# Performance work log

Measured on AMD Instinct MI355X. Metric: run time of the kernel, lower is better.

Reference implementation:

```python
import jax, jax.numpy as jnp
import numpy as np

HIDDEN = 1024
HEADS = 16
DEPTH = HIDDEN // HEADS  # 64
B, S = 1, 2048  # batch must be 1: E is built with shape (heads, B*S, depth) and the skew reshape assumes B*S == S


def setup_inputs() -> dict:
    key = jax.random.key(0)
    ks = jax.random.split(key, 6)
    std = 0.02
    x = jax.random.normal(ks[0], (B, S, HIDDEN), dtype=jnp.float32)
    c_attn_w = jax.random.normal(ks[1], (HIDDEN, 3 * HIDDEN), dtype=jnp.float32) * std
    c_attn_b = jnp.zeros((1, 3 * HIDDEN), dtype=jnp.float32)
    c_proj_w = jax.random.normal(ks[2], (HIDDEN, HIDDEN), dtype=jnp.float32) * std
    c_proj_b = jnp.zeros((1, HIDDEN), dtype=jnp.float32)
    # GlorotUniform for E of shape (heads, B*S, depth)
    limit = float(np.sqrt(6.0 / (B * S + DEPTH)))
    E = jax.random.uniform(ks[3], (HEADS, B * S, DEPTH), dtype=jnp.float32,
                           minval=-limit, maxval=limit)
    return {"x": x, "c_attn_w": c_attn_w, "c_attn_b": c_attn_b,
            "c_proj_w": c_proj_w, "c_proj_b": c_proj_b, "E": E}


def _split_heads(t):
    # [B,S,H] -> [B,heads,S,depth]
    b, s, h = t.shape
    return t.reshape(b, s, HEADS, h // HEADS).transpose(0, 2, 1, 3)


def _relative_attention(q, E):
    # Transformer-XL style skewing. q: [B,heads,S,depth], E: [heads,B*S,depth]
    b, h, s, d = q.shape
    q_ = q.transpose(1, 0, 2, 3).reshape(h, b * s, d)
    rel = jnp.einsum('hnd,hmd->hnm', q_, E)            # [h, B*S, B*S]
    rel = rel.reshape(h, b, s, s)
    rel = jnp.pad(rel, ((0, 0), (0, 0), (0, 0), (1, 0)))  # pad left on last dim
    rel = rel.reshape(h, b, s + 1, s)[:, :, 1:]            # skew
    return rel.transpose(1, 0, 2, 3)                       # [B,heads,S,S]


def reference(x, c_attn_w, c_attn_b, c_proj_w, c_proj_b, E):
    b, s, hidden = x.shape
    qkv = x @ c_attn_w + c_attn_b                      # [B,S,3H]
    q, k, v = jnp.split(qkv, 3, axis=2)
    q, k, v = _split_heads(q), _split_heads(k), _split_heads(v)  # [B,h,S,d]

    w = jnp.einsum('bhqd,bhkd->bhqk', q, k)            # raw scores
    w = w + _relative_attention(q, E)
    w = w * jax.lax.rsqrt(jnp.asarray(DEPTH, w.dtype))  # scale applied after rel bias

    # causal mask: 1 in lower triangle (i >= j - ns + nd, nd == ns == S)
    i = jnp.arange(s)[:, None]
    j = jnp.arange(s)[None, :]
    bmask = (i >= j).astype(w.dtype)[None, None]        # [1,1,S,S]
    w = w * bmask - 10000.0 * (1.0 - bmask)

    a = jax.nn.softmax(w, axis=-1)                      # dropout is identity at inference
    ctx = jnp.einsum('bhqk,bhkd->bhqd', a, v)
    ctx = ctx.transpose(0, 2, 1, 3).reshape(b, s, hidden)  # merge heads
    out = ctx @ c_proj_w + c_proj_b
    return out
```

## Files before the change

kernel.cpp:

```cpp
#include <hip/hip_runtime.h>
#include <math.h>

#define SEQ  2048
#define NH   16
#define DEP  64
#define HID  1024

typedef __attribute__((ext_vector_type(8))) short s16x8;
typedef __attribute__((ext_vector_type(4))) float f32x4;

#define MFMA16(a, b, c) __builtin_amdgcn_mfma_f32_16x16x32_bf16(a, b, c, 0, 0, 0)
#define GLDS16(g, l)                                                           \
  __builtin_amdgcn_global_load_lds(                                            \
      (const __attribute__((address_space(1))) void*)(g),                      \
      (__attribute__((address_space(3))) void*)(l), 16, 0, 0)

__device__ __forceinline__ ushort f2b(float f) {
  union { float f; unsigned u; } x; x.f = f;
  unsigned r = (x.u + 0x7fff + ((x.u >> 16) & 1)) >> 16;
  return (ushort)r;
}
__device__ __forceinline__ float b2f(ushort u) {
  union { unsigned u; float f; } x; x.u = ((unsigned)u) << 16;
  return x.f;
}

__global__ __launch_bounds__(256) void prep(
    const float* __restrict__ x, ushort* __restrict__ xb,
    const float* __restrict__ E, ushort* __restrict__ Eb,
    const float* __restrict__ Wa, ushort* __restrict__ Wat,
    const float* __restrict__ Wp, ushort* __restrict__ Wpt) {
  const int bid = blockIdx.x, t = threadIdx.x;
  if (bid < 1024) {
    __shared__ float Ls[64 * 68];
    const float* in; ushort* out; int C, tile;
    if (bid < 768) { in = Wa; out = Wat; C = 3072; tile = bid; }
    else           { in = Wp; out = Wpt; C = 1024; tile = bid - 768; }
    const int ntx = C / 64;
    const int n0 = (tile % ntx) * 64, k0 = (tile / ntx) * 64;
    const int r = t >> 4, c4 = t & 15;
    #pragma unroll
    for (int p = 0; p < 4; p++) {
      float4 v = *(const float4*)&in[(size_t)(k0 + r + 16 * p) * C + n0 + c4 * 4];
      *(float4*)&Ls[(r + 16 * p) * 68 + c4 * 4] = v;
    }
    __syncthreads();
    #pragma unroll
    for (int p = 0; p < 4; p++) {
      int rw = r + 16 * p;
      ushort4 o;
      o.x = f2b(Ls[(c4 * 4 + 0) * 68 + rw]);
      o.y = f2b(Ls[(c4 * 4 + 1) * 68 + rw]);
      o.z = f2b(Ls[(c4 * 4 + 2) * 68 + rw]);
      o.w = f2b(Ls[(c4 * 4 + 3) * 68 + rw]);
      *(ushort4*)&out[(size_t)(n0 + rw) * 1024 + k0 + c4 * 4] = o;
    }
  } else {
    const int id = bid - 1024;
    #pragma unroll
    for (int rep = 0; rep < 4; rep++) {
      int i = id * 256 + t + rep * 262144;
      const float* src; ushort* dst; int k;
      if (i < 524288) { src = x; dst = xb; k = i; }
      else            { src = E; dst = Eb; k = i - 524288; }
      float4 v = *(const float4*)&src[(size_t)k * 4];
      ushort4 o = {f2b(v.x), f2b(v.y), f2b(v.z), f2b(v.w)};
      *(ushort4*)&dst[(size_t)k * 4] = o;
    }
  }
}

template <int MODE>
__global__ __launch_bounds__(256, 3) void gemm_mfma(
    const ushort* __restrict__ A, const ushort* __restrict__ Bt,
    const float* __restrict__ bias, int N, int K,
    ushort* __restrict__ qd, ushort* __restrict__ kd, ushort* __restrict__ vt,
    float* __restrict__ Cout) {
  __shared__ ushort As[2][64 * 64];
  __shared__ ushort Bs[2][128 * 64];
  const int t = threadIdx.x, l = t & 63, w = t >> 6;
  const int lr = l & 15, quad = l >> 4;
  const int row8 = l >> 3;
  const int chunk = (l & 7) ^ ((l >> 3) & 7);
  const int m0 = blockIdx.y * 64, n0 = blockIdx.x * 128;
  const int wr = (w >> 1) * 32, wc = (w & 1) * 64;
  f32x4 acc[2][4] = {};
  const ushort* gA = A + (size_t)m0 * K + chunk * 8;
  const ushort* gB = Bt + (size_t)n0 * K + chunk * 8;

  auto issue = [&](int buf, int k0) {
    #pragma unroll
    for (int g = 0; g < 2; g++) {
      int r = 16 * w + 8 * g + row8;
      GLDS16(gA + (size_t)r * K + k0, &As[buf][(16 * w + 8 * g) * 64]);
    }
    #pragma unroll
    for (int g = 0; g < 4; g++) {
      int r = 32 * w + 8 * g + row8;
      GLDS16(gB + (size_t)r * K + k0, &Bs[buf][(32 * w + 8 * g) * 64]);
    }
  };

  issue(0, 0);
  const int nsteps = K / 64;
  for (int s = 0; s < nsteps; s++) {
    __syncthreads();
    if (s + 1 < nsteps) issue((s + 1) & 1, (s + 1) * 64);
    const char* as_ = (const char*)As[s & 1];
    const char* bs_ = (const char*)Bs[s & 1];
    s16x8 af[2][2], bf[4][2];
    #pragma unroll
    for (int i = 0; i < 2; i++)
      #pragma unroll
      for (int hh = 0; hh < 2; hh++)
        af[i][hh] = *(const s16x8*)(as_ + (wr + 16 * i + lr) * 128 +
                                    (((4 * hh + quad) ^ (lr & 7)) * 16));
    #pragma unroll
    for (int j = 0; j < 4; j++)
      #pragma unroll
      for (int hh = 0; hh < 2; hh++)
        bf[j][hh] = *(const s16x8*)(bs_ + (wc + 16 * j + lr) * 128 +
                                    (((4 * hh + quad) ^ (lr & 7)) * 16));
    #pragma unroll
    for (int i = 0; i < 2; i++)
      #pragma unroll
      for (int j = 0; j < 4; j++) {
        acc[i][j] = MFMA16(af[i][0], bf[j][0], acc[i][j]);
        acc[i][j] = MFMA16(af[i][1], bf[j][1], acc[i][j]);
      }
  }

  #pragma unroll
  for (int i = 0; i < 2; i++) {
    #pragma unroll
    for (int j = 0; j < 4; j++) {
      const int colg = n0 + wc + 16 * j + lr;
      const float bb = bias[colg];
      const int rowg0 = m0 + wr + 16 * i + 4 * quad;
      if (MODE == 0) {
        const int part = colg >> 10, hh = (colg >> 6) & 15, d = colg & 63;
        if (part == 2) {
          ushort4 ov;
          ov.x = f2b(acc[i][j][0] + bb);
          ov.y = f2b(acc[i][j][1] + bb);
          ov.z = f2b(acc[i][j][2] + bb);
          ov.w = f2b(acc[i][j][3] + bb);
          *(ushort4*)&vt[((size_t)hh * 64 + d) * SEQ + rowg0] = ov;
        } else {
          ushort* dst = part == 0 ? qd : kd;
          const float sc = part == 0 ? 0.125f : 1.0f;
          #pragma unroll
          for (int r = 0; r < 4; r++)
            dst[((size_t)hh * SEQ + rowg0 + r) * 64 + d] = f2b((acc[i][j][r] + bb) * sc);
        }
      } else {
        #pragma unroll
        for (int r = 0; r < 4; r++)
          Cout[(size_t)(rowg0 + r) * N + colg] = acc[i][j][r] + bb;
      }
    }
  }
}

__global__ __launch_bounds__(256, 2) void attn_mfma(
    const ushort* __restrict__ qw, const ushort* __restrict__ kw,
    const ushort* __restrict__ vT, const ushort* __restrict__ Ebf,
    ushort* __restrict__ ctx, ushort* __restrict__ pa_o,
    float* __restrict__ pa_l) {
  __shared__ ushort KT[2][64 * 64];
  __shared__ ushort VS[2][64 * 64];
  __shared__ ushort EB[2][128 * 64];
  __shared__ ushort PB[4][16 * 72];
  const int t = threadIdx.x, l = t & 63, w = t >> 6;
  const int lr = l & 15, quad = l >> 4;
  const int row8 = l >> 3;
  const int chunk = (l & 7) ^ ((l >> 3) & 7);
  const int h = blockIdx.y;
  const int p = blockIdx.x >> 1, half = blockIdx.x & 1;
  const int i0A = 64 * p, i0B = 64 * (31 - p);

  int ph_i0[2], ph_k0[2], ph_k1[2], nph, tot;
  bool ph_diag[2], ph_dir[2];
  if (half == 0) {
    ph_i0[0] = i0A; ph_k0[0] = 0; ph_k1[0] = p + 1;  ph_diag[0] = true;  ph_dir[0] = true;
    ph_i0[1] = i0B; ph_k0[1] = 0; ph_k1[1] = 16 - p; ph_diag[1] = false; ph_dir[1] = false;
    nph = 2; tot = 17;
  } else {
    ph_i0[0] = i0B; ph_k0[0] = 16 - p; ph_k1[0] = 32 - p; ph_diag[0] = true; ph_dir[0] = false;
    ph_i0[1] = 0; ph_k0[1] = 0; ph_k1[1] = 0; ph_diag[1] = false; ph_dir[1] = false;
    nph = 1; tot = 16;
  }

  const ushort* kwh = kw + (size_t)h * SEQ * 64;
  const ushort* vgh = vT + (size_t)h * 64 * SEQ;
  const ushort* egh = Ebf + (size_t)h * SEQ * 64;

  auto issue = [&](int buf, int i0_, int j0) {
    const int m0 = 1984 - i0_ + j0;
    const ushort* kb = kwh + (size_t)j0 * 64 + chunk * 8;
    const ushort* vb = vgh + j0 + chunk * 8;
    #pragma unroll
    for (int g = 0; g < 2; g++) {
      int r = 16 * w + 8 * g + row8;
      GLDS16(kb + (size_t)r * 64, &KT[buf][(16 * w + 8 * g) * 64]);
      GLDS16(vb + (size_t)r * SEQ, &VS[buf][(16 * w + 8 * g) * 64]);
    }
    #pragma unroll
    for (int g = 0; g < 4; g++) {
      int r = m0 + 32 * w + 8 * g + row8;
      if (r > SEQ - 1) r = SEQ - 1;
      GLDS16(egh + (size_t)r * 64 + chunk * 8, &EB[buf][(32 * w + 8 * g) * 64]);
    }
  };

  int pi = 0, kt = ph_k0[0];
  issue(0, ph_i0[0], kt * 64);

  s16x8 aq0, aq1;
  {
    const ushort* qg = qw + ((size_t)h * SEQ + ph_i0[0] + 16 * w) * 64;
    aq0 = *(const s16x8*)(qg + lr * 64 + quad * 8);
    aq1 = *(const s16x8*)(qg + lr * 64 + 32 + quad * 8);
  }

  f32x4 o[4] = {};
  float li[4] = {0.f, 0.f, 0.f, 0.f};
  f32x4 rtc = {};

  for (int s = 0; s < tot; s++) {
    __syncthreads();

    const int i0 = ph_i0[pi];
    const bool first = (kt == ph_k0[pi]);
    const bool last = (kt == ph_k1[pi] - 1);
    const bool diag = ph_diag[pi] && last;

    {
      int npi = pi, nkt = kt + 1;
      bool have = true;
      if (nkt == ph_k1[pi]) {
        if (pi + 1 < nph) { npi = pi + 1; nkt = ph_k0[npi]; } else have = false;
      }
      if (have) issue((s + 1) & 1, ph_i0[npi], nkt * 64);
    }

    const char* KTc = (const char*)KT[s & 1];
    const char* VSc = (const char*)VS[s & 1];
    const char* EBc = (const char*)EB[s & 1];

    f32x4 s4[4];
    #pragma unroll
    for (int b = 0; b < 4; b++) {
      const int row = 16 * b + lr;
      s16x8 bk0 = *(const s16x8*)(KTc + row * 128 + ((quad ^ (lr & 7)) * 16));
      s16x8 bk1 = *(const s16x8*)(KTc + row * 128 + (((4 + quad) ^ (lr & 7)) * 16));
      f32x4 z = {};
      z = MFMA16(aq0, bk0, z);
      z = MFMA16(aq1, bk1, z);
      s4[b] = z;
    }

    {
      const int ebase = 48 - 16 * w;
      f32x4 rt[5];
      if (first) {
        const int row = ebase + lr;
        s16x8 e0 = *(const s16x8*)(EBc + row * 128 + ((quad ^ (lr & 7)) * 16));
        s16x8 e1 = *(const s16x8*)(EBc + row * 128 + (((4 + quad) ^ (lr & 7)) * 16));
        f32x4 z = {};
        z = MFMA16(aq0, e0, z);
        z = MFMA16(aq1, e1, z);
        rt[0] = z;
      } else {
        rt[0] = rtc;
      }
      #pragma unroll
      for (int b = 1; b < 5; b++) {
        const int row = ebase + 16 * b + lr;
        s16x8 e0 = *(const s16x8*)(EBc + row * 128 + ((quad ^ (lr & 7)) * 16));
        s16x8 e1 = *(const s16x8*)(EBc + row * 128 + (((4 + quad) ^ (lr & 7)) * 16));
        f32x4 z = {};
        z = MFMA16(aq0, e0, z);
        z = MFMA16(aq1, e1, z);
        rt[b] = z;
      }
      rtc = rt[4];
      #pragma unroll
      for (int b = 0; b < 4; b++)
        #pragma unroll
        for (int r = 0; r < 4; r++) {
          int ti = 4 * quad + r;
          int u = lr - ti + 15;
          int src = (u & 15) | (l & 48);
          float v0 = __shfl(rt[b][r], src);
          float v1 = __shfl(rt[b + 1][r], src);
          s4[b][r] += (u < 16) ? v0 : v1;
        }
    }

    if (diag) {
      #pragma unroll
      for (int b = 0; b < 4; b++)
        #pragma unroll
        for (int r = 0; r < 4; r++) {
          int ii = 16 * w + 4 * quad + r;
          if (16 * b + lr > ii) s4[b][r] = -10000.0f;
        }
    }

    #pragma unroll
    for (int b = 0; b < 4; b++)
      #pragma unroll
      for (int r = 0; r < 4; r++) {
        float pp = __expf(s4[b][r]);
        s4[b][r] = pp;
        li[r] += pp;
      }

    {
      char* Pw = (char*)PB[w];
      #pragma unroll
      for (int b = 0; b < 4; b++)
        #pragma unroll
        for (int r = 0; r < 4; r++)
          *(ushort*)(Pw + (4 * quad + r) * 144 + (16 * b + lr) * 2) = f2b(s4[b][r]);
      s16x8 pa0 = *(const s16x8*)(Pw + lr * 144 + quad * 16);
      s16x8 pa1 = *(const s16x8*)(Pw + lr * 144 + 64 + quad * 16);
      #pragma unroll
      for (int dc = 0; dc < 4; dc++) {
        const int row = 16 * dc + lr;
        s16x8 bv0 = *(const s16x8*)(VSc + row * 128 + ((quad ^ (lr & 7)) * 16));
        s16x8 bv1 = *(const s16x8*)(VSc + row * 128 + (((4 + quad) ^ (lr & 7)) * 16));
        o[dc] = MFMA16(pa0, bv0, o[dc]);
        o[dc] = MFMA16(pa1, bv1, o[dc]);
      }
    }

    if (last) {
      float lsum[4];
      #pragma unroll
      for (int r = 0; r < 4; r++) {
        float v = li[r];
        v += __shfl_xor(v, 1);
        v += __shfl_xor(v, 2);
        v += __shfl_xor(v, 4);
        v += __shfl_xor(v, 8);
        lsum[r] = v;
      }
      if (ph_dir[pi]) {
        #pragma unroll
        for (int r = 0; r < 4; r++) {
          float inv = 1.0f / lsum[r];
          #pragma unroll
          for (int dc = 0; dc < 4; dc++) {
            int row = i0 + 16 * w + 4 * quad + r;
            int col = h * 64 + 16 * dc + lr;
            ctx[(size_t)row * HID + col] = f2b(o[dc][r] * inv);
          }
        }
      } else {
        ushort* po = pa_o + (((size_t)(h * 16 + p) * 2 + half) * 4096);
        float* pl = pa_l + (((size_t)(h * 16 + p) * 2 + half) * 64);
        #pragma unroll
        for (int r = 0; r < 4; r++) {
          int row = 16 * w + 4 * quad + r;
          #pragma unroll
          for (int dc = 0; dc < 4; dc++)
            po[row * 64 + 16 * dc + lr] = f2b(o[dc][r]);
          if (lr == 0) pl[row] = lsum[r];
        }
      }
      #pragma unroll
      for (int dc = 0; dc < 4; dc++) o[dc] = (f32x4){0.f, 0.f, 0.f, 0.f};
      #pragma unroll
      for (int r = 0; r < 4; r++) li[r] = 0.f;
      if (pi + 1 < nph) {
        const ushort* qg = qw + ((size_t)h * SEQ + ph_i0[pi + 1] + 16 * w) * 64;
        aq0 = *(const s16x8*)(qg + lr * 64 + quad * 8);
        aq1 = *(const s16x8*)(qg + lr * 64 + 32 + quad * 8);
      }
    }

    if (kt + 1 == ph_k1[pi]) { pi++; kt = (pi < nph) ? ph_k0[pi] : 0; }
    else kt++;
  }
}

__global__ __launch_bounds__(256) void merge_p(const ushort* __restrict__ pa_o,
                                               const float* __restrict__ pa_l,
                                               ushort* __restrict__ ctx) {
  const int p = blockIdx.x, h = blockIdx.y, t = threadIdx.x;
  const int row = t >> 2, seg = t & 3;
  const ushort* o0 = pa_o + ((size_t)(h * 16 + p) * 2 + 0) * 4096;
  const ushort* o1 = pa_o + ((size_t)(h * 16 + p) * 2 + 1) * 4096;
  const float* l0 = pa_l + ((size_t)(h * 16 + p) * 2 + 0) * 64;
  const float* l1 = pa_l + ((size_t)(h * 16 + p) * 2 + 1) * 64;
  const float inv = 1.0f / (l0[row] + l1[row]);
  const int i0b = 64 * (31 - p);
  #pragma unroll
  for (int g = 0; g < 2; g++) {
    ushort a[8], b[8], r[8];
    *(int4*)a = *(const int4*)&o0[row * 64 + seg * 16 + g * 8];
    *(int4*)b = *(const int4*)&o1[row * 64 + seg * 16 + g * 8];
    #pragma unroll
    for (int j = 0; j < 8; j++) r[j] = f2b((b2f(a[j]) + b2f(b[j])) * inv);
    *(int4*)&ctx[(size_t)(i0b + row) * HID + h * 64 + seg * 16 + g * 8] = *(int4*)r;
  }
}

extern "C" void kernel_launch(void* const* d_in, const int* in_sizes, int n_in,
                              void* d_out, int out_size, void* d_ws, size_t ws_size,
                              hipStream_t stream) {
  (void)in_sizes; (void)n_in; (void)out_size; (void)ws_size;
  const float* x  = (const float*)d_in[0];
  const float* Wa = (const float*)d_in[1];
  const float* ba = (const float*)d_in[2];
  const float* Wp = (const float*)d_in[3];
  const float* bp = (const float*)d_in[4];
  const float* E  = (const float*)d_in[5];
  float* out = (float*)d_out;

  ushort* xb  = (ushort*)d_ws;
  ushort* ctx = xb;
  ushort* Wat = xb + (size_t)2 * 1024 * 1024;
  ushort* Wpt = Wat + (size_t)3 * 1024 * 1024;
  ushort* Ebf = Wpt + (size_t)1024 * 1024;
  ushort* qwp = Ebf + (size_t)2 * 1024 * 1024;
  ushort* kwp = qwp + (size_t)2 * 1024 * 1024;
  ushort* vTp = kwp + (size_t)2 * 1024 * 1024;
  ushort* pa_o = Wat;
  float*  pa_l = (float*)(Wat + (size_t)2 * 1024 * 1024);

  prep<<<2048, 256, 0, stream>>>(x, xb, E, Ebf, Wa, Wat, Wp, Wpt);
  gemm_mfma<0><<<dim3(24, 32), 256, 0, stream>>>(xb, Wat, ba, 3 * HID, HID,
                                                 qwp, kwp, vTp, nullptr);
  attn_mfma<<<dim3(32, NH), 256, 0, stream>>>(qwp, kwp, vTp, Ebf, ctx,
                                              pa_o, pa_l);
  merge_p<<<dim3(16, NH), 256, 0, stream>>>(pa_o, pa_l, ctx);
  gemm_mfma<1><<<dim3(8, 32), 256, 0, stream>>>(ctx, Wpt, bp, HID, HID,
                                                nullptr, nullptr, nullptr, out);
}
```

Before: 160.1 us.

## Reuse overlapping E rows via ring buffer and narrow output-projection GEMM tiles

The attention kernel now keeps E tiles in a 4-slot ring of 64-row slots. Consecutive key tiles share 64 of their 128 skewed E rows, so each step loads only one new 64-row slot instead of the full 128 rows, with two slots loaded when a new phase starts. Separately, the GEMM is templated on tile width, and the output projection uses 64-wide tiles to launch twice as many blocks and fill more CUs. The slot indexing and phase-change logic add complexity, and it could break if the row overlap assumption fails.

```diff
diff --git a/kernel.cpp b/kernel.cpp
--- a/kernel.cpp
+++ b/kernel.cpp
@@ -70,21 +70,22 @@
   }
 }
 
-template <int MODE>
+template <int MODE, int BN>
 __global__ __launch_bounds__(256, 3) void gemm_mfma(
     const ushort* __restrict__ A, const ushort* __restrict__ Bt,
     const float* __restrict__ bias, int N, int K,
     ushort* __restrict__ qd, ushort* __restrict__ kd, ushort* __restrict__ vt,
     float* __restrict__ Cout) {
+  constexpr int NJ = BN / 32;
   __shared__ ushort As[2][64 * 64];
-  __shared__ ushort Bs[2][128 * 64];
+  __shared__ ushort Bs[2][BN * 64];
   const int t = threadIdx.x, l = t & 63, w = t >> 6;
   const int lr = l & 15, quad = l >> 4;
   const int row8 = l >> 3;
   const int chunk = (l & 7) ^ ((l >> 3) & 7);
-  const int m0 = blockIdx.y * 64, n0 = blockIdx.x * 128;
-  const int wr = (w >> 1) * 32, wc = (w & 1) * 64;
-  f32x4 acc[2][4] = {};
+  const int m0 = blockIdx.y * 64, n0 = blockIdx.x * BN;
+  const int wr = (w >> 1) * 32, wc = (w & 1) * (BN / 2);
+  f32x4 acc[2][NJ] = {};
   const ushort* gA = A + (size_t)m0 * K + chunk * 8;
   const ushort* gB = Bt + (size_t)n0 * K + chunk * 8;
 
@@ -95,9 +96,9 @@
       GLDS16(gA + (size_t)r * K + k0, &As[buf][(16 * w + 8 * g) * 64]);
     }
     #pragma unroll
-    for (int g = 0; g < 4; g++) {
-      int r = 32 * w + 8 * g + row8;
-      GLDS16(gB + (size_t)r * K + k0, &Bs[buf][(32 * w + 8 * g) * 64]);
+    for (int g = 0; g < BN / 32; g++) {
+      int r = (BN / 4) * w + 8 * g + row8;
+      GLDS16(gB + (size_t)r * K + k0, &Bs[buf][((BN / 4) * w + 8 * g) * 64]);
     }
   };
 
@@ -108,7 +109,7 @@
     if (s + 1 < nsteps) issue((s + 1) & 1, (s + 1) * 64);
     const char* as_ = (const char*)As[s & 1];
     const char* bs_ = (const char*)Bs[s & 1];
-    s16x8 af[2][2], bf[4][2];
+    s16x8 af[2][2], bf[NJ][2];
     #pragma unroll
     for (int i = 0; i < 2; i++)
       #pragma unroll
@@ -116,7 +117,7 @@
         af[i][hh] = *(const s16x8*)(as_ + (wr + 16 * i + lr) * 128 +
                                     (((4 * hh + quad) ^ (lr & 7)) * 16));
     #pragma unroll
-    for (int j = 0; j < 4; j++)
+    for (int j = 0; j < NJ; j++)
       #pragma unroll
       for (int hh = 0; hh < 2; hh++)
         bf[j][hh] = *(const s16x8*)(bs_ + (wc + 16 * j + lr) * 128 +
@@ -124,7 +125,7 @@
     #pragma unroll
     for (int i = 0; i < 2; i++)
       #pragma unroll
-      for (int j = 0; j < 4; j++) {
+      for (int j = 0; j < NJ; j++) {
         acc[i][j] = MFMA16(af[i][0], bf[j][0], acc[i][j]);
         acc[i][j] = MFMA16(af[i][1], bf[j][1], acc[i][j]);
       }
@@ -133,7 +134,7 @@
   #pragma unroll
   for (int i = 0; i < 2; i++) {
     #pragma unroll
-    for (int j = 0; j < 4; j++) {
+    for (int j = 0; j < NJ; j++) {
       const int colg = n0 + wc + 16 * j + lr;
       const float bb = bias[colg];
       const int rowg0 = m0 + wr + 16 * i + 4 * quad;
@@ -169,7 +170,7 @@
     float* __restrict__ pa_l) {
   __shared__ ushort KT[2][64 * 64];
   __shared__ ushort VS[2][64 * 64];
-  __shared__ ushort EB[2][128 * 64];
+  __shared__ ushort EB[4][64 * 64];
   __shared__ ushort PB[4][16 * 72];
   const int t = threadIdx.x, l = t & 63, w = t >> 6;
   const int lr = l & 15, quad = l >> 4;
@@ -195,8 +196,7 @@
   const ushort* vgh = vT + (size_t)h * 64 * SEQ;
   const ushort* egh = Ebf + (size_t)h * SEQ * 64;
 
-  auto issue = [&](int buf, int i0_, int j0) {
-    const int m0 = 1984 - i0_ + j0;
+  auto issue_kv = [&](int buf, int j0) {
     const ushort* kb = kwh + (size_t)j0 * 64 + chunk * 8;
     const ushort* vb = vgh + j0 + chunk * 8;
     #pragma unroll
@@ -205,16 +205,23 @@
       GLDS16(kb + (size_t)r * 64, &KT[buf][(16 * w + 8 * g) * 64]);
       GLDS16(vb + (size_t)r * SEQ, &VS[buf][(16 * w + 8 * g) * 64]);
     }
-    #pragma unroll
-    for (int g = 0; g < 4; g++) {
-      int r = m0 + 32 * w + 8 * g + row8;
+  };
+  auto issue_e = [&](int slot, int r0) {
+    #pragma unroll
+    for (int g = 0; g < 2; g++) {
+      int r = r0 + 16 * w + 8 * g + row8;
       if (r > SEQ - 1) r = SEQ - 1;
-      GLDS16(egh + (size_t)r * 64 + chunk * 8, &EB[buf][(32 * w + 8 * g) * 64]);
+      GLDS16(egh + (size_t)r * 64 + chunk * 8, &EB[slot][(16 * w + 8 * g) * 64]);
     }
   };
 
-  int pi = 0, kt = ph_k0[0];
-  issue(0, ph_i0[0], kt * 64);
+  int pi = 0, kt = ph_k0[0], ebs = 0;
+  {
+    const int m0 = 1984 - ph_i0[0] + kt * 64;
+    issue_kv(0, kt * 64);
+    issue_e(0, m0);
+    issue_e(1, m0 + 64);
+  }
 
   s16x8 aq0, aq1;
   {
@@ -235,18 +242,37 @@
     const bool last = (kt == ph_k1[pi] - 1);
     const bool diag = ph_diag[pi] && last;
 
+    int ebs_next = ebs;
     {
       int npi = pi, nkt = kt + 1;
-      bool have = true;
+      bool have = true, newph = false;
       if (nkt == ph_k1[pi]) {
-        if (pi + 1 < nph) { npi = pi + 1; nkt = ph_k0[npi]; } else have = false;
-      }
-      if (have) issue((s + 1) & 1, ph_i0[npi], nkt * 64);
+        if (pi + 1 < nph) { npi = pi + 1; nkt = ph_k0[npi]; newph = true; }
+        else have = false;
+      }
+      if (have) {
+        issue_kv((s + 1) & 1, nkt * 64);
+        const int m0n = 1984 - ph_i0[npi] + nkt * 64;
+        if (newph) {
+          issue_e((ebs + 2) & 3, m0n);
+          issue_e((ebs + 3) & 3, m0n + 64);
+          ebs_next = (ebs + 2) & 3;
+        } else {
+          issue_e((ebs + 2) & 3, m0n + 64);
+          ebs_next = (ebs + 1) & 3;
+        }
+      }
     }
 
     const char* KTc = (const char*)KT[s & 1];
     const char* VSc = (const char*)VS[s & 1];
-    const char* EBc = (const char*)EB[s & 1];
+
+    auto eb_frag = [&](int row, s16x8& e0, s16x8& e1) {
+      const char* e_ = (const char*)EB[(ebs + (row >> 6)) & 3];
+      const int rb = (row & 63) * 128;
+      e0 = *(const s16x8*)(e_ + rb + ((quad ^ (lr & 7)) * 16));
+      e1 = *(const s16x8*)(e_ + rb + (((4 + quad) ^ (lr & 7)) * 16));
+    };
 
     f32x4 s4[4];
     #pragma unroll
@@ -264,9 +290,8 @@
       const int ebase = 48 - 16 * w;
       f32x4 rt[5];
       if (first) {
-        const int row = ebase + lr;
-        s16x8 e0 = *(const s16x8*)(EBc + row * 128 + ((quad ^ (lr & 7)) * 16));
-        s16x8 e1 = *(const s16x8*)(EBc + row * 128 + (((4 + quad) ^ (lr & 7)) * 16));
+        s16x8 e0, e1;
+        eb_frag(ebase + lr, e0, e1);
         f32x4 z = {};
         z = MFMA16(aq0, e0, z);
         z = MFMA16(aq1, e1, z);
@@ -276,9 +301,8 @@
       }
       #pragma unroll
       for (int b = 1; b < 5; b++) {
-        const int row = ebase + 16 * b + lr;
-        s16x8 e0 = *(const s16x8*)(EBc + row * 128 + ((quad ^ (lr & 7)) * 16));
-        s16x8 e1 = *(const s16x8*)(EBc + row * 128 + (((4 + quad) ^ (lr & 7)) * 16));
+        s16x8 e0, e1;
+        eb_frag(ebase + 16 * b + lr, e0, e1);
         f32x4 z = {};
         z = MFMA16(aq0, e0, z);
         z = MFMA16(aq1, e1, z);
@@ -383,6 +407,7 @@
 
     if (kt + 1 == ph_k1[pi]) { pi++; kt = (pi < nph) ? ph_k0[pi] : 0; }
     else kt++;
+    ebs = ebs_next;
   }
 }
 
@@ -432,11 +457,11 @@
   float*  pa_l = (float*)(Wat + (size_t)2 * 1024 * 1024);
 
   prep<<<2048, 256, 0, stream>>>(x, xb, E, Ebf, Wa, Wat, Wp, Wpt);
-  gemm_mfma<0><<<dim3(24, 32), 256, 0, stream>>>(xb, Wat, ba, 3 * HID, HID,
-                                                 qwp, kwp, vTp, nullptr);
+  gemm_mfma<0, 128><<<dim3(24, 32), 256, 0, stream>>>(xb, Wat, ba, 3 * HID, HID,
+                                                      qwp, kwp, vTp, nullptr);
   attn_mfma<<<dim3(32, NH), 256, 0, stream>>>(qwp, kwp, vTp, Ebf, ctx,
                                               pa_o, pa_l);
   merge_p<<<dim3(16, NH), 256, 0, stream>>>(pa_o, pa_l, ctx);
-  gemm_mfma<1><<<dim3(8, 32), 256, 0, stream>>>(ctx, Wpt, bp, HID, HID,
-                                                nullptr, nullptr, nullptr, out);
-}
+  gemm_mfma<1, 64><<<dim3(16, 32), 256, 0, stream>>>(ctx, Wpt, bp, HID, HID,
+                                                     nullptr, nullptr, nullptr, out);
+}
```

Result: faster. 156.8 us (-2.1%).

## Drop LDS staging in attention, read K/V/E fragments directly from global

Applied to the files above, without the earlier changes.

The attention kernel no longer double-buffers K, V and E tiles through LDS with block barriers. Each wave now loads its MFMA operand fragments straight from global memory, which frees LDS, raises the occupancy hint to 3 and remaps block indices so heads interleave across the grid. The projection GEMM gets its own kernel with 64x64 tiles, doubling its block count, and the skew shuffle is restructured to issue each shuffle once instead of twice. The risk is redundant global/L2 traffic, since waves in a block reload the same K and V rows and E loads lose coalescing, and the loads are no longer prefetched ahead of use.

```diff
diff --git a/kernel.cpp b/kernel.cpp
--- a/kernel.cpp
+++ b/kernel.cpp
@@ -70,12 +70,10 @@
   }
 }
 
-template <int MODE>
-__global__ __launch_bounds__(256, 3) void gemm_mfma(
+__global__ __launch_bounds__(256, 3) void gemm_qkv(
     const ushort* __restrict__ A, const ushort* __restrict__ Bt,
     const float* __restrict__ bias, int N, int K,
-    ushort* __restrict__ qd, ushort* __restrict__ kd, ushort* __restrict__ vt,
-    float* __restrict__ Cout) {
+    ushort* __restrict__ qd, ushort* __restrict__ kd, ushort* __restrict__ vt) {
   __shared__ ushort As[2][64 * 64];
   __shared__ ushort Bs[2][128 * 64];
   const int t = threadIdx.x, l = t & 63, w = t >> 6;
@@ -137,46 +135,104 @@
       const int colg = n0 + wc + 16 * j + lr;
       const float bb = bias[colg];
       const int rowg0 = m0 + wr + 16 * i + 4 * quad;
-      if (MODE == 0) {
-        const int part = colg >> 10, hh = (colg >> 6) & 15, d = colg & 63;
-        if (part == 2) {
-          ushort4 ov;
-          ov.x = f2b(acc[i][j][0] + bb);
-          ov.y = f2b(acc[i][j][1] + bb);
-          ov.z = f2b(acc[i][j][2] + bb);
-          ov.w = f2b(acc[i][j][3] + bb);
-          *(ushort4*)&vt[((size_t)hh * 64 + d) * SEQ + rowg0] = ov;
-        } else {
-          ushort* dst = part == 0 ? qd : kd;
-          const float sc = part == 0 ? 0.125f : 1.0f;
-          #pragma unroll
-          for (int r = 0; r < 4; r++)
-            dst[((size_t)hh * SEQ + rowg0 + r) * 64 + d] = f2b((acc[i][j][r] + bb) * sc);
-        }
+      const int part = colg >> 10, hh = (colg >> 6) & 15, d = colg & 63;
+      if (part == 2) {
+        ushort4 ov;
+        ov.x = f2b(acc[i][j][0] + bb);
+        ov.y = f2b(acc[i][j][1] + bb);
+        ov.z = f2b(acc[i][j][2] + bb);
+        ov.w = f2b(acc[i][j][3] + bb);
+        *(ushort4*)&vt[((size_t)hh * 64 + d) * SEQ + rowg0] = ov;
       } else {
+        ushort* dst = part == 0 ? qd : kd;
+        const float sc = part == 0 ? 0.125f : 1.0f;
         #pragma unroll
         for (int r = 0; r < 4; r++)
-          Cout[(size_t)(rowg0 + r) * N + colg] = acc[i][j][r] + bb;
-      }
-    }
-  }
-}
-
-__global__ __launch_bounds__(256, 2) void attn_mfma(
+          dst[((size_t)hh * SEQ + rowg0 + r) * 64 + d] = f2b((acc[i][j][r] + bb) * sc);
+      }
+    }
+  }
+}
+
+__global__ __launch_bounds__(256, 3) void gemm_proj(
+    const ushort* __restrict__ A, const ushort* __restrict__ Bt,
+    const float* __restrict__ bias, float* __restrict__ Cout) {
+  const int K = HID, N = HID;
+  __shared__ ushort As[2][64 * 64];
+  __shared__ ushort Bs[2][64 * 64];
+  const int t = threadIdx.x, l = t & 63, w = t >> 6;
+  const int lr = l & 15, quad = l >> 4;
+  const int row8 = l >> 3;
+  const int chunk = (l & 7) ^ ((l >> 3) & 7);
+  const int m0 = blockIdx.y * 64, n0 = blockIdx.x * 64;
+  const int wr = (w >> 1) * 32, wc = (w & 1) * 32;
+  f32x4 acc[2][2] = {};
+  const ushort* gA = A + (size_t)m0 * K + chunk * 8;
+  const ushort* gB = Bt + (size_t)n0 * K + chunk * 8;
+
+  auto issue = [&](int buf, int k0) {
+    #pragma unroll
+    for (int g = 0; g < 2; g++) {
+      int r = 16 * w + 8 * g;
+      GLDS16(gA + (size_t)(r + row8) * K + k0, &As[buf][r * 64]);
+      GLDS16(gB + (size_t)(r + row8) * K + k0, &Bs[buf][r * 64]);
+    }
+  };
+
+  issue(0, 0);
+  const int nsteps = K / 64;
+  for (int s = 0; s < nsteps; s++) {
+    __syncthreads();
+    if (s + 1 < nsteps) issue((s + 1) & 1, (s + 1) * 64);
+    const char* as_ = (const char*)As[s & 1];
+    const char* bs_ = (const char*)Bs[s & 1];
+    s16x8 af[2][2], bf[2][2];
+    #pragma unroll
+    for (int i = 0; i < 2; i++)
+      #pragma unroll
+      for (int hh = 0; hh < 2; hh++)
+        af[i][hh] = *(const s16x8*)(as_ + (wr + 16 * i + lr) * 128 +
+                                    (((4 * hh + quad) ^ (lr & 7)) * 16));
+    #pragma unroll
+    for (int j = 0; j < 2; j++)
+      #pragma unroll
+      for (int hh = 0; hh < 2; hh++)
+        bf[j][hh] = *(const s16x8*)(bs_ + (wc + 16 * j + lr) * 128 +
+                                    (((4 * hh + quad) ^ (lr & 7)) * 16));
+    #pragma unroll
+    for (int i = 0; i < 2; i++)
+      #pragma unroll
+      for (int j = 0; j < 2; j++) {
+        acc[i][j] = MFMA16(af[i][0], bf[j][0], acc[i][j]);
+        acc[i][j] = MFMA16(af[i][1], bf[j][1], acc[i][j]);
+      }
+  }
+
+  #pragma unroll
+  for (int i = 0; i < 2; i++)
+    #pragma unroll
+    for (int j = 0; j < 2; j++) {
+      const int colg = n0 + wc + 16 * j + lr;
+      const float bb = bias[colg];
+      const int rowg0 = m0 + wr + 16 * i + 4 * quad;
+      #pragma unroll
+      for (int r = 0; r < 4; r++)
+        Cout[(size_t)(rowg0 + r) * N + colg] = acc[i][j][r] + bb;
+    }
+}
+
+__global__ __launch_bounds__(256, 3) void attn_mfma(
     const ushort* __restrict__ qw, const ushort* __restrict__ kw,
     const ushort* __restrict__ vT, const ushort* __restrict__ Ebf,
     ushort* __restrict__ ctx, ushort* __restrict__ pa_o,
     float* __restrict__ pa_l) {
-  __shared__ ushort KT[2][64 * 64];
-  __shared__ ushort VS[2][64 * 64];
-  __shared__ ushort EB[2][128 * 64];
   __shared__ ushort PB[4][16 * 72];
   const int t = threadIdx.x, l = t & 63, w = t >> 6;
   const int lr = l & 15, quad = l >> 4;
-  const int row8 = l >> 3;
-  const int chunk = (l & 7) ^ ((l >> 3) & 7);
-  const int h = blockIdx.y;
-  const int p = blockIdx.x >> 1, half = blockIdx.x & 1;
+  const int bid = blockIdx.x;
+  const int h = (bid & 7) * 2 + ((bid >> 3) >> 5);
+  const int s32 = (bid >> 3) & 31;
+  const int p = s32 >> 1, half = s32 & 1;
   const int i0A = 64 * p, i0B = 64 * (31 - p);
 
   int ph_i0[2], ph_k0[2], ph_k1[2], nph, tot;
@@ -195,27 +251,6 @@
   const ushort* vgh = vT + (size_t)h * 64 * SEQ;
   const ushort* egh = Ebf + (size_t)h * SEQ * 64;
 
-  auto issue = [&](int buf, int i0_, int j0) {
-    const int m0 = 1984 - i0_ + j0;
-    const ushort* kb = kwh + (size_t)j0 * 64 + chunk * 8;
-    const ushort* vb = vgh + j0 + chunk * 8;
-    #pragma unroll
-    for (int g = 0; g < 2; g++) {
-      int r = 16 * w + 8 * g + row8;
-      GLDS16(kb + (size_t)r * 64, &KT[buf][(16 * w + 8 * g) * 64]);
-      GLDS16(vb + (size_t)r * SEQ, &VS[buf][(16 * w + 8 * g) * 64]);
-    }
-    #pragma unroll
-    for (int g = 0; g < 4; g++) {
-      int r = m0 + 32 * w + 8 * g + row8;
-      if (r > SEQ - 1) r = SEQ - 1;
-      GLDS16(egh + (size_t)r * 64 + chunk * 8, &EB[buf][(32 * w + 8 * g) * 64]);
-    }
-  };
-
-  int pi = 0, kt = ph_k0[0];
-  issue(0, ph_i0[0], kt * 64);
-
   s16x8 aq0, aq1;
   {
     const ushort* qg = qw + ((size_t)h * SEQ + ph_i0[0] + 16 * w) * 64;
@@ -226,34 +261,22 @@
   f32x4 o[4] = {};
   float li[4] = {0.f, 0.f, 0.f, 0.f};
   f32x4 rtc = {};
+  int pi = 0, kt = ph_k0[0];
 
   for (int s = 0; s < tot; s++) {
-    __syncthreads();
-
     const int i0 = ph_i0[pi];
     const bool first = (kt == ph_k0[pi]);
     const bool last = (kt == ph_k1[pi] - 1);
     const bool diag = ph_diag[pi] && last;
-
-    {
-      int npi = pi, nkt = kt + 1;
-      bool have = true;
-      if (nkt == ph_k1[pi]) {
-        if (pi + 1 < nph) { npi = pi + 1; nkt = ph_k0[npi]; } else have = false;
-      }
-      if (have) issue((s + 1) & 1, ph_i0[npi], nkt * 64);
-    }
-
-    const char* KTc = (const char*)KT[s & 1];
-    const char* VSc = (const char*)VS[s & 1];
-    const char* EBc = (const char*)EB[s & 1];
+    const int j0 = kt * 64;
+    const int m0 = 1984 - i0 + j0;
 
     f32x4 s4[4];
     #pragma unroll
     for (int b = 0; b < 4; b++) {
-      const int row = 16 * b + lr;
-      s16x8 bk0 = *(const s16x8*)(KTc + row * 128 + ((quad ^ (lr & 7)) * 16));
-      s16x8 bk1 = *(const s16x8*)(KTc + row * 128 + (((4 + quad) ^ (lr & 7)) * 16));
+      const ushort* kr = kwh + (size_t)(j0 + 16 * b + lr) * 64 + quad * 8;
+      s16x8 bk0 = *(const s16x8*)kr;
+      s16x8 bk1 = *(const s16x8*)(kr + 32);
       f32x4 z = {};
       z = MFMA16(aq0, bk0, z);
       z = MFMA16(aq1, bk1, z);
@@ -262,11 +285,17 @@
 
     {
       const int ebase = 48 - 16 * w;
+      auto eb_frag = [&](int row, s16x8& e0, s16x8& e1) {
+        int g = m0 + row;
+        if (g > SEQ - 1) g = SEQ - 1;
+        const ushort* er = egh + (size_t)g * 64 + quad * 8;
+        e0 = *(const s16x8*)er;
+        e1 = *(const s16x8*)(er + 32);
+      };
       f32x4 rt[5];
       if (first) {
-        const int row = ebase + lr;
-        s16x8 e0 = *(const s16x8*)(EBc + row * 128 + ((quad ^ (lr & 7)) * 16));
-        s16x8 e1 = *(const s16x8*)(EBc + row * 128 + (((4 + quad) ^ (lr & 7)) * 16));
+        s16x8 e0, e1;
+        eb_frag(ebase + lr, e0, e1);
         f32x4 z = {};
         z = MFMA16(aq0, e0, z);
         z = MFMA16(aq1, e1, z);
@@ -276,9 +305,8 @@
       }
       #pragma unroll
       for (int b = 1; b < 5; b++) {
-        const int row = ebase + 16 * b + lr;
-        s16x8 e0 = *(const s16x8*)(EBc + row * 128 + ((quad ^ (lr & 7)) * 16));
-        s16x8 e1 = *(const s16x8*)(EBc + row * 128 + (((4 + quad) ^ (lr & 7)) * 16));
+        s16x8 e0, e1;
+        eb_frag(ebase + 16 * b + lr, e0, e1);
         f32x4 z = {};
         z = MFMA16(aq0, e0, z);
         z = MFMA16(aq1, e1, z);
@@ -286,16 +314,20 @@
       }
       rtc = rt[4];
       #pragma unroll
-      for (int b = 0; b < 4; b++)
-        #pragma unroll
-        for (int r = 0; r < 4; r++) {
-          int ti = 4 * quad + r;
-          int u = lr - ti + 15;
-          int src = (u & 15) | (l & 48);
-          float v0 = __shfl(rt[b][r], src);
-          float v1 = __shfl(rt[b + 1][r], src);
-          s4[b][r] += (u < 16) ? v0 : v1;
-        }
+      for (int r = 0; r < 4; r++) {
+        const int ti = 4 * quad + r;
+        const int u = lr - ti + 15;
+        const int src = (u & 15) | (l & 48);
+        const float sh0 = __shfl(rt[0][r], src);
+        const float sh1 = __shfl(rt[1][r], src);
+        const float sh2 = __shfl(rt[2][r], src);
+        const float sh3 = __shfl(rt[3][r], src);
+        const float sh4 = __shfl(rt[4][r], src);
+        s4[0][r] += (u < 16) ? sh0 : sh1;
+        s4[1][r] += (u < 16) ? sh1 : sh2;
+        s4[2][r] += (u < 16) ? sh2 : sh3;
+        s4[3][r] += (u < 16) ? sh3 : sh4;
+      }
     }
 
     if (diag) {
@@ -328,9 +360,9 @@
       s16x8 pa1 = *(const s16x8*)(Pw + lr * 144 + 64 + quad * 16);
       #pragma unroll
       for (int dc = 0; dc < 4; dc++) {
-        const int row = 16 * dc + lr;
-        s16x8 bv0 = *(const s16x8*)(VSc + row * 128 + ((quad ^ (lr & 7)) * 16));
-        s16x8 bv1 = *(const s16x8*)(VSc + row * 128 + (((4 + quad) ^ (lr & 7)) * 16));
+        const ushort* vr = vgh + (size_t)(16 * dc + lr) * SEQ + j0 + quad * 8;
+        s16x8 bv0 = *(const s16x8*)vr;
+        s16x8 bv1 = *(const s16x8*)(vr + 32);
         o[dc] = MFMA16(pa0, bv0, o[dc]);
         o[dc] = MFMA16(pa1, bv1, o[dc]);
       }
@@ -432,11 +464,9 @@
   float*  pa_l = (float*)(Wat + (size_t)2 * 1024 * 1024);
 
   prep<<<2048, 256, 0, stream>>>(x, xb, E, Ebf, Wa, Wat, Wp, Wpt);
-  gemm_mfma<0><<<dim3(24, 32), 256, 0, stream>>>(xb, Wat, ba, 3 * HID, HID,
-                                                 qwp, kwp, vTp, nullptr);
-  attn_mfma<<<dim3(32, NH), 256, 0, stream>>>(qwp, kwp, vTp, Ebf, ctx,
-                                              pa_o, pa_l);
+  gemm_qkv<<<dim3(24, 32), 256, 0, stream>>>(xb, Wat, ba, 3 * HID, HID,
+                                             qwp, kwp, vTp);
+  attn_mfma<<<512, 256, 0, stream>>>(qwp, kwp, vTp, Ebf, ctx, pa_o, pa_l);
   merge_p<<<dim3(16, NH), 256, 0, stream>>>(pa_o, pa_l, ctx);
-  gemm_mfma<1><<<dim3(8, 32), 256, 0, stream>>>(ctx, Wpt, bp, HID, HID,
-                                                nullptr, nullptr, nullptr, out);
-}
+  gemm_proj<<<dim3(16, 32), 256, 0, stream>>>(ctx, Wpt, bp, out);
+}
```

Measured after the change: 213.2 us. 1.33x slower.
